# Kernel optimization log

Measured on AMD Instinct MI355X. Metric: run time of the kernel, lower is better.

## Reference

```python
import jax, jax.numpy as jnp
import numpy as np

SYM_LIST = np.array([12, 15, 18, 19, 20], dtype=np.int32)   # symmetric class ids (dataset.get_sym_list())
SELECT_ID = np.arange(1, 31, dtype=np.int32)                 # self.select_id = [1..30]
STEP = 20                                                     # pixel subsampling stride
SCORING_WEIGHT = 0.01


def quat_to_mat(q):
    """Exact translation of get_loss.quaternion_matrix. q: [..., 4] -> [..., 3, 3]."""
    q0, q1, q2, q3 = q[..., 0], q[..., 1], q[..., 2], q[..., 3]
    R = jnp.stack([
        1.0 - 2.0 * (q2 ** 2 + q3 ** 2), 2.0 * q1 * q2 - 2.0 * q0 * q3, 2.0 * q0 * q2 + 2.0 * q1 * q3,
        2.0 * q1 * q2 + 2.0 * q3 * q0, 1.0 - 2.0 * (q1 ** 2 + q3 ** 2), -2.0 * q0 * q1 + 2.0 * q2 * q3,
        -2.0 * q0 * q2 + 2.0 * q1 * q3, 2.0 * q0 * q1 + 2.0 * q2 * q3, 1.0 - 2.0 * (q1 ** 2 + q2 ** 2),
    ], axis=-1)
    return R.reshape(q.shape[:-1] + (3, 3))


def setup_inputs() -> dict:
    key = jax.random.key(0)
    ks = jax.random.split(key, 7)
    bs, h, w, P = 8, 64, 64, 400
    pred_r = jax.random.normal(ks[0], (bs, 4, h, w), jnp.float32)
    pred_t = jax.random.normal(ks[1], (bs, 3, h, w), jnp.float32) * 0.1
    pred_score = jax.random.uniform(ks[2], (bs, h, w), jnp.float32, 1e-3, 1.0)
    gt_r = jax.random.normal(ks[3], (bs, 3, 3), jnp.float32)
    gt_t = jax.random.normal(ks[4], (bs, 3), jnp.float32) * 0.1
    cls_ids = jax.random.randint(ks[5], (bs,), 0, 30, jnp.int32)
    model_xyz = jax.random.normal(ks[6], (bs, 3, P), jnp.float32) * 0.05
    return {"pred_r": pred_r, "pred_t": pred_t, "pred_score": pred_score,
            "gt_r": gt_r, "gt_t": gt_t, "cls_ids": cls_ids, "model_xyz": model_xyz}


def reference(pred_r, pred_t, pred_score, gt_r, gt_t, cls_ids, model_xyz):
    bs, _, h, w = pred_r.shape
    hw = h * w
    # per-pixel quaternion normalization
    pred_r = pred_r / jnp.linalg.norm(pred_r, axis=1, keepdims=True)
    pr = pred_r.reshape(bs, 4, hw)
    pt = pred_t.reshape(bs, 3, hw)
    ps = pred_score.reshape(bs, hw)
    # static strided subsampling of valid pixels (full mask -> every STEP-th pixel)
    V = hw // STEP
    idx = jnp.arange(V) * STEP
    pr = pr[:, :, idx]                 # [bs,4,V]
    pt = pt[:, :, idx]                 # [bs,3,V]
    ps = ps[:, idx]                    # [bs,V]
    R_pre = quat_to_mat(jnp.moveaxis(pr, 1, 2))                       # [bs,V,3,3]
    # transformed model points per valid pixel
    pred = jnp.einsum('bvij,bjp->bvip', R_pre, model_xyz) \
        + jnp.moveaxis(pt, 1, 2)[..., None]                           # [bs,V,3,P]
    gt = jnp.einsum('bij,bjp->bip', gt_r, model_xyz) + gt_t[..., None]  # [bs,3,P]
    # ADD: same-index point distances
    add = jnp.mean(jnp.linalg.norm(pred - gt[:, None], axis=2), axis=2)  # [bs,V]
    # ADD-S: nearest-neighbor (knn_one_point + gather == min over gt points)
    pn = jnp.sum(pred ** 2, axis=2)                                    # [bs,V,P]
    gn = jnp.sum(gt ** 2, axis=1)                                      # [bs,P]
    cross = jnp.einsum('bvip,biq->bvpq', pred, gt)                     # [bs,V,P,P]
    d2 = pn[..., None] + gn[:, None, None, :] - 2.0 * cross
    adds = jnp.mean(jnp.sqrt(jnp.maximum(jnp.min(d2, axis=-1), 0.0)), axis=2)  # [bs,V]
    is_sym = jnp.isin(cls_ids, jnp.asarray(SYM_LIST))                  # [bs]
    add_ij = jnp.where(is_sym[:, None], adds, add)                     # [bs,V]
    valid = jnp.isin(cls_ids + 1, jnp.asarray(SELECT_ID))              # cls+1 in select_id
    sub_value = jnp.where(valid, jnp.mean(add_ij, axis=1), 0.0)
    sub_loss = jnp.where(valid,
                         jnp.mean(add_ij * ps - SCORING_WEIGHT * jnp.log(ps), axis=1), 0.0)
    gadd_loss = jnp.mean(sub_loss)
    gadd = jnp.mean(sub_value)
    bad = jnp.isinf(gadd_loss) | jnp.isnan(gadd_loss)
    gadd_loss = jnp.where(bad, 0.0, gadd_loss)
    return gadd_loss + 0.0 * gadd
```

## Files before the change

kernel.cpp:

```cpp
#include <hip/hip_runtime.h>
#include <math.h>

#define NP 400
#define NV 204
#define STEP 20
#define HW 4096
#define BS 8
#define NBLK (NV * BS)

__global__ __launch_bounds__(512) void partial_kernel(
    const float* __restrict__ pred_r,
    const float* __restrict__ pred_t,
    const float* __restrict__ pred_score,
    const float* __restrict__ gt_r,
    const float* __restrict__ gt_t,
    const int*   __restrict__ cls_ids,
    const float* __restrict__ model_xyz,
    float* __restrict__ partials)
{
    const int v   = blockIdx.x;
    const int b   = blockIdx.y;
    const int tid = threadIdx.x;
    const int pix = v * STEP;

    __shared__ float4 s_g[NP];
    __shared__ float  s_part[8];

    const int   cls = cls_ids[b];
    const bool  sym = (cls==12)||(cls==15)||(cls==18)||(cls==19)||(cls==20);
    const bool  valid = (cls+1 >= 1) && (cls+1 <= 30);

    const float* mb = model_xyz + (size_t)b * 3 * NP;

    if (tid < NP) {
        const float g00 = gt_r[b*9+0], g01 = gt_r[b*9+1], g02 = gt_r[b*9+2];
        const float g10 = gt_r[b*9+3], g11 = gt_r[b*9+4], g12 = gt_r[b*9+5];
        const float g20 = gt_r[b*9+6], g21 = gt_r[b*9+7], g22 = gt_r[b*9+8];
        const float gtx = gt_t[b*3+0], gty = gt_t[b*3+1], gtz = gt_t[b*3+2];
        float mx = mb[tid], my = mb[NP+tid], mz = mb[2*NP+tid];
        s_g[tid] = make_float4(g00*mx + g01*my + g02*mz + gtx,
                               g10*mx + g11*my + g12*mz + gty,
                               g20*mx + g21*my + g22*mz + gtz, 0.0f);
    }

    float q0 = pred_r[((size_t)b*4+0)*HW + pix];
    float q1 = pred_r[((size_t)b*4+1)*HW + pix];
    float q2 = pred_r[((size_t)b*4+2)*HW + pix];
    float q3 = pred_r[((size_t)b*4+3)*HW + pix];
    {
        float inv = 1.0f / sqrtf(q0*q0 + q1*q1 + q2*q2 + q3*q3);
        q0 *= inv; q1 *= inv; q2 *= inv; q3 *= inv;
    }
    const float R00 = 1.0f - 2.0f*(q2*q2 + q3*q3);
    const float R01 = 2.0f*q1*q2 - 2.0f*q0*q3;
    const float R02 = 2.0f*q0*q2 + 2.0f*q1*q3;
    const float R10 = 2.0f*q1*q2 + 2.0f*q3*q0;
    const float R11 = 1.0f - 2.0f*(q1*q1 + q3*q3);
    const float R12 = -2.0f*q0*q1 + 2.0f*q2*q3;
    const float R20 = -2.0f*q0*q2 + 2.0f*q1*q3;
    const float R21 = 2.0f*q0*q1 + 2.0f*q2*q3;
    const float R22 = 1.0f - 2.0f*(q1*q1 + q2*q2);

    const float ptx = pred_t[((size_t)b*3+0)*HW + pix];
    const float pty = pred_t[((size_t)b*3+1)*HW + pix];
    const float ptz = pred_t[((size_t)b*3+2)*HW + pix];

    __syncthreads();

    float local = 0.0f;
    if (tid < NP) {
        const int p = tid;
        float mx = mb[p], my = mb[NP+p], mz = mb[2*NP+p];
        float px = R00*mx + R01*my + R02*mz + ptx;
        float py = R10*mx + R11*my + R12*mz + pty;
        float pz = R20*mx + R21*my + R22*mz + ptz;
        float d2;
        if (sym) {
            float m0 = 3.4e38f, m1 = 3.4e38f, m2 = 3.4e38f, m3 = 3.4e38f;
            for (int q = 0; q < NP; q += 4) {
                float4 g0 = s_g[q+0], g1 = s_g[q+1], g2 = s_g[q+2], g3 = s_g[q+3];
                float dx0 = px-g0.x, dy0 = py-g0.y, dz0 = pz-g0.z;
                float dx1 = px-g1.x, dy1 = py-g1.y, dz1 = pz-g1.z;
                float dx2 = px-g2.x, dy2 = py-g2.y, dz2 = pz-g2.z;
                float dx3 = px-g3.x, dy3 = py-g3.y, dz3 = pz-g3.z;
                m0 = fminf(m0, dx0*dx0 + dy0*dy0 + dz0*dz0);
                m1 = fminf(m1, dx1*dx1 + dy1*dy1 + dz1*dz1);
                m2 = fminf(m2, dx2*dx2 + dy2*dy2 + dz2*dz2);
                m3 = fminf(m3, dx3*dx3 + dy3*dy3 + dz3*dz3);
            }
            d2 = fminf(fminf(m0, m1), fminf(m2, m3));
        } else {
            float4 g = s_g[p];
            float dx = px-g.x, dy = py-g.y, dz = pz-g.z;
            d2 = dx*dx + dy*dy + dz*dz;
        }
        local = sqrtf(d2);
    }

    #pragma unroll
    for (int off = 32; off > 0; off >>= 1)
        local += __shfl_down(local, off, 64);
    const int wave = tid >> 6;
    if ((tid & 63) == 0) s_part[wave] = local;
    __syncthreads();
    if (tid == 0) {
        float tot = 0.0f;
        #pragma unroll
        for (int w = 0; w < 8; ++w) tot += s_part[w];
        float mean = tot * (1.0f / NP);
        float ps   = pred_score[(size_t)b*HW + pix];
        float c = 0.0f;
        if (valid)
            c = (mean * ps - 0.01f * logf(ps)) * (1.0f / NBLK);
        partials[b * NV + v] = c;
    }
}

__global__ __launch_bounds__(256) void finalize_kernel(
    const float* __restrict__ partials, float* __restrict__ out)
{
    __shared__ float s_part[4];
    const int tid = threadIdx.x;
    float local = 0.0f;
    for (int i = tid; i < NBLK; i += 256) local += partials[i];
    #pragma unroll
    for (int off = 32; off > 0; off >>= 1)
        local += __shfl_down(local, off, 64);
    if ((tid & 63) == 0) s_part[tid >> 6] = local;
    __syncthreads();
    if (tid == 0) {
        float vv = s_part[0] + s_part[1] + s_part[2] + s_part[3];
        if (isnan(vv) || isinf(vv)) vv = 0.0f;
        out[0] = vv;
    }
}

extern "C" void kernel_launch(void* const* d_in, const int* in_sizes, int n_in,
                              void* d_out, int out_size, void* d_ws, size_t ws_size,
                              hipStream_t stream) {
    const float* pred_r     = (const float*)d_in[0];
    const float* pred_t     = (const float*)d_in[1];
    const float* pred_score = (const float*)d_in[2];
    const float* gt_r       = (const float*)d_in[3];
    const float* gt_t       = (const float*)d_in[4];
    const int*   cls_ids    = (const int*)d_in[5];
    const float* model_xyz  = (const float*)d_in[6];
    float* out      = (float*)d_out;
    float* partials = (float*)d_ws;

    dim3 grid(NV, BS);
    partial_kernel<<<grid, 512, 0, stream>>>(pred_r, pred_t, pred_score,
                                             gt_r, gt_t, cls_ids, model_xyz, partials);
    finalize_kernel<<<1, 256, 0, stream>>>(partials, out);
}
```

Measured before the change: 71.74 us.

## Process two model points per thread with SoA shared layout and 256-thread blocks

Shrinks each block from 512 to 256 threads, so each thread now handles two predicted points and every vectorized shared-memory load of ground-truth points is reused across both. The ground-truth points are stored as separate x/y/z arrays, so four points come in with three float4 loads and no padding lane. Before, 112 of the 512 threads did no work. The finalize kernel now reads the partials as float4. The cost is lower occupancy per block and a thread-load imbalance, since only 144 of the 256 threads have a second point.

```diff
diff --git a/kernel.cpp b/kernel.cpp
--- a/kernel.cpp
+++ b/kernel.cpp
@@ -8,7 +8,7 @@
 #define BS 8
 #define NBLK (NV * BS)
 
-__global__ __launch_bounds__(512) void partial_kernel(
+__global__ __launch_bounds__(256) void partial_kernel(
     const float* __restrict__ pred_r,
     const float* __restrict__ pred_t,
     const float* __restrict__ pred_score,
@@ -23,24 +23,27 @@
     const int tid = threadIdx.x;
     const int pix = v * STEP;
 
-    __shared__ float4 s_g[NP];
-    __shared__ float  s_part[8];
+    __shared__ float s_gx[NP], s_gy[NP], s_gz[NP];
+    __shared__ float s_part[4];
 
     const int   cls = cls_ids[b];
     const bool  sym = (cls==12)||(cls==15)||(cls==18)||(cls==19)||(cls==20);
     const bool  valid = (cls+1 >= 1) && (cls+1 <= 30);
+    const bool  has2 = (tid < NP - 256);
 
     const float* mb = model_xyz + (size_t)b * 3 * NP;
 
-    if (tid < NP) {
+    {
         const float g00 = gt_r[b*9+0], g01 = gt_r[b*9+1], g02 = gt_r[b*9+2];
         const float g10 = gt_r[b*9+3], g11 = gt_r[b*9+4], g12 = gt_r[b*9+5];
         const float g20 = gt_r[b*9+6], g21 = gt_r[b*9+7], g22 = gt_r[b*9+8];
         const float gtx = gt_t[b*3+0], gty = gt_t[b*3+1], gtz = gt_t[b*3+2];
-        float mx = mb[tid], my = mb[NP+tid], mz = mb[2*NP+tid];
-        s_g[tid] = make_float4(g00*mx + g01*my + g02*mz + gtx,
-                               g10*mx + g11*my + g12*mz + gty,
-                               g20*mx + g21*my + g22*mz + gtz, 0.0f);
+        for (int q = tid; q < NP; q += 256) {
+            float mx = mb[q], my = mb[NP+q], mz = mb[2*NP+q];
+            s_gx[q] = g00*mx + g01*my + g02*mz + gtx;
+            s_gy[q] = g10*mx + g11*my + g12*mz + gty;
+            s_gz[q] = g20*mx + g21*my + g22*mz + gtz;
+        }
     }
 
     float q0 = pred_r[((size_t)b*4+0)*HW + pix];
@@ -67,35 +70,55 @@
 
     __syncthreads();
 
-    float local = 0.0f;
-    if (tid < NP) {
-        const int p = tid;
-        float mx = mb[p], my = mb[NP+p], mz = mb[2*NP+p];
-        float px = R00*mx + R01*my + R02*mz + ptx;
-        float py = R10*mx + R11*my + R12*mz + pty;
-        float pz = R20*mx + R21*my + R22*mz + ptz;
-        float d2;
-        if (sym) {
-            float m0 = 3.4e38f, m1 = 3.4e38f, m2 = 3.4e38f, m3 = 3.4e38f;
-            for (int q = 0; q < NP; q += 4) {
-                float4 g0 = s_g[q+0], g1 = s_g[q+1], g2 = s_g[q+2], g3 = s_g[q+3];
-                float dx0 = px-g0.x, dy0 = py-g0.y, dz0 = pz-g0.z;
-                float dx1 = px-g1.x, dy1 = py-g1.y, dz1 = pz-g1.z;
-                float dx2 = px-g2.x, dy2 = py-g2.y, dz2 = pz-g2.z;
-                float dx3 = px-g3.x, dy3 = py-g3.y, dz3 = pz-g3.z;
-                m0 = fminf(m0, dx0*dx0 + dy0*dy0 + dz0*dz0);
-                m1 = fminf(m1, dx1*dx1 + dy1*dy1 + dz1*dz1);
-                m2 = fminf(m2, dx2*dx2 + dy2*dy2 + dz2*dz2);
-                m3 = fminf(m3, dx3*dx3 + dy3*dy3 + dz3*dz3);
+    const int p0 = tid;
+    const int p1 = has2 ? tid + 256 : tid;
+    float mx0 = mb[p0], my0 = mb[NP+p0], mz0 = mb[2*NP+p0];
+    float mx1 = mb[p1], my1 = mb[NP+p1], mz1 = mb[2*NP+p1];
+    const float px0 = R00*mx0 + R01*my0 + R02*mz0 + ptx;
+    const float py0 = R10*mx0 + R11*my0 + R12*mz0 + pty;
+    const float pz0 = R20*mx0 + R21*my0 + R22*mz0 + ptz;
+    const float px1 = R00*mx1 + R01*my1 + R02*mz1 + ptx;
+    const float py1 = R10*mx1 + R11*my1 + R12*mz1 + pty;
+    const float pz1 = R20*mx1 + R21*my1 + R22*mz1 + ptz;
+
+    float d2_0, d2_1;
+    if (sym) {
+        float a0 = 3.4e38f, a1 = 3.4e38f, a2 = 3.4e38f, a3 = 3.4e38f;
+        float b0 = 3.4e38f, b1 = 3.4e38f, b2 = 3.4e38f, b3 = 3.4e38f;
+        for (int q = 0; q < NP; q += 4) {
+            const float4 gx = *reinterpret_cast<const float4*>(&s_gx[q]);
+            const float4 gy = *reinterpret_cast<const float4*>(&s_gy[q]);
+            const float4 gz = *reinterpret_cast<const float4*>(&s_gz[q]);
+            {
+                float dx = px0-gx.x, dy = py0-gy.x, dz = pz0-gz.x;
+                a0 = fminf(a0, dx*dx + dy*dy + dz*dz);
+                dx = px0-gx.y; dy = py0-gy.y; dz = pz0-gz.y;
+                a1 = fminf(a1, dx*dx + dy*dy + dz*dz);
+                dx = px0-gx.z; dy = py0-gy.z; dz = pz0-gz.z;
+                a2 = fminf(a2, dx*dx + dy*dy + dz*dz);
+                dx = px0-gx.w; dy = py0-gy.w; dz = pz0-gz.w;
+                a3 = fminf(a3, dx*dx + dy*dy + dz*dz);
             }
-            d2 = fminf(fminf(m0, m1), fminf(m2, m3));
-        } else {
-            float4 g = s_g[p];
-            float dx = px-g.x, dy = py-g.y, dz = pz-g.z;
-            d2 = dx*dx + dy*dy + dz*dz;
+            {
+                float dx = px1-gx.x, dy = py1-gy.x, dz = pz1-gz.x;
+                b0 = fminf(b0, dx*dx + dy*dy + dz*dz);
+                dx = px1-gx.y; dy = py1-gy.y; dz = pz1-gz.y;
+                b1 = fminf(b1, dx*dx + dy*dy + dz*dz);
+                dx = px1-gx.z; dy = py1-gy.z; dz = pz1-gz.z;
+                b2 = fminf(b2, dx*dx + dy*dy + dz*dz);
+                dx = px1-gx.w; dy = py1-gy.w; dz = pz1-gz.w;
+                b3 = fminf(b3, dx*dx + dy*dy + dz*dz);
+            }
         }
-        local = sqrtf(d2);
+        d2_0 = fminf(fminf(a0, a1), fminf(a2, a3));
+        d2_1 = fminf(fminf(b0, b1), fminf(b2, b3));
+    } else {
+        float dx = px0 - s_gx[p0], dy = py0 - s_gy[p0], dz = pz0 - s_gz[p0];
+        d2_0 = dx*dx + dy*dy + dz*dz;
+        dx = px1 - s_gx[p1]; dy = py1 - s_gy[p1]; dz = pz1 - s_gz[p1];
+        d2_1 = dx*dx + dy*dy + dz*dz;
     }
+    float local = sqrtf(d2_0) + (has2 ? sqrtf(d2_1) : 0.0f);
 
     #pragma unroll
     for (int off = 32; off > 0; off >>= 1)
@@ -104,9 +127,7 @@
     if ((tid & 63) == 0) s_part[wave] = local;
     __syncthreads();
     if (tid == 0) {
-        float tot = 0.0f;
-        #pragma unroll
-        for (int w = 0; w < 8; ++w) tot += s_part[w];
+        float tot  = s_part[0] + s_part[1] + s_part[2] + s_part[3];
         float mean = tot * (1.0f / NP);
         float ps   = pred_score[(size_t)b*HW + pix];
         float c = 0.0f;
@@ -121,8 +142,12 @@
 {
     __shared__ float s_part[4];
     const int tid = threadIdx.x;
+    const float4* p4 = reinterpret_cast<const float4*>(partials);
     float local = 0.0f;
-    for (int i = tid; i < NBLK; i += 256) local += partials[i];
+    for (int i = tid; i < NBLK / 4; i += 256) {
+        float4 vv = p4[i];
+        local += vv.x + vv.y + vv.z + vv.w;
+    }
     #pragma unroll
     for (int off = 32; off > 0; off >>= 1)
         local += __shfl_down(local, off, 64);
@@ -149,7 +174,7 @@
     float* partials = (float*)d_ws;
 
     dim3 grid(NV, BS);
-    partial_kernel<<<grid, 512, 0, stream>>>(pred_r, pred_t, pred_score,
+    partial_kernel<<<grid, 256, 0, stream>>>(pred_r, pred_t, pred_score,
                                              gt_r, gt_t, cls_ids, model_xyz, partials);
     finalize_kernel<<<1, 256, 0, stream>>>(partials, out);
 }
```

Result: faster. 69.99 us (-2.4%).

## Register-tile nearest-neighbor search with expanded-norm distances across four waves

Applied to the files above, without the earlier changes.

Shrinks blocks to 256 threads. Each lane now holds 7 predicted points in registers, and each wave scans a quarter of the ground-truth points using the expanded distance form -2p·g + |g|^2, computed as three FMAs. Per-wave minima are merged through shared memory. This cuts shared-memory loads per distance and reduces the ALU work in the symmetric kNN loop. In exchange it adds register pressure, padding lanes that do clamped redundant work, and an extra barrier. The finalize kernel is also switched to float4 loads.

```diff
diff --git a/kernel.cpp b/kernel.cpp
--- a/kernel.cpp
+++ b/kernel.cpp
@@ -7,8 +7,9 @@
 #define HW 4096
 #define BS 8
 #define NBLK (NV * BS)
+#define NJ 7
 
-__global__ __launch_bounds__(512) void partial_kernel(
+__global__ __launch_bounds__(256) void partial_kernel(
     const float* __restrict__ pred_r,
     const float* __restrict__ pred_t,
     const float* __restrict__ pred_score,
@@ -18,13 +19,15 @@
     const float* __restrict__ model_xyz,
     float* __restrict__ partials)
 {
-    const int v   = blockIdx.x;
-    const int b   = blockIdx.y;
-    const int tid = threadIdx.x;
-    const int pix = v * STEP;
+    const int v    = blockIdx.x;
+    const int b    = blockIdx.y;
+    const int tid  = threadIdx.x;
+    const int lane = tid & 63;
+    const int wave = tid >> 6;
+    const int pix  = v * STEP;
 
     __shared__ float4 s_g[NP];
-    __shared__ float  s_part[8];
+    __shared__ float  s_wmin[4][NP];
 
     const int   cls = cls_ids[b];
     const bool  sym = (cls==12)||(cls==15)||(cls==18)||(cls==19)||(cls==20);
@@ -32,15 +35,18 @@
 
     const float* mb = model_xyz + (size_t)b * 3 * NP;
 
-    if (tid < NP) {
+    {
         const float g00 = gt_r[b*9+0], g01 = gt_r[b*9+1], g02 = gt_r[b*9+2];
         const float g10 = gt_r[b*9+3], g11 = gt_r[b*9+4], g12 = gt_r[b*9+5];
         const float g20 = gt_r[b*9+6], g21 = gt_r[b*9+7], g22 = gt_r[b*9+8];
         const float gtx = gt_t[b*3+0], gty = gt_t[b*3+1], gtz = gt_t[b*3+2];
-        float mx = mb[tid], my = mb[NP+tid], mz = mb[2*NP+tid];
-        s_g[tid] = make_float4(g00*mx + g01*my + g02*mz + gtx,
-                               g10*mx + g11*my + g12*mz + gty,
-                               g20*mx + g21*my + g22*mz + gtz, 0.0f);
+        for (int q = tid; q < NP; q += 256) {
+            float mx = mb[q], my = mb[NP+q], mz = mb[2*NP+q];
+            float gx = g00*mx + g01*my + g02*mz + gtx;
+            float gy = g10*mx + g11*my + g12*mz + gty;
+            float gz = g20*mx + g21*my + g22*mz + gtz;
+            s_g[q] = make_float4(gx, gy, gz, gx*gx + gy*gy + gz*gz);
+        }
     }
 
     float q0 = pred_r[((size_t)b*4+0)*HW + pix];
@@ -65,54 +71,85 @@
     const float pty = pred_t[((size_t)b*3+1)*HW + pix];
     const float ptz = pred_t[((size_t)b*3+2)*HW + pix];
 
+    float px[NJ], py[NJ], pz[NJ], nx[NJ], ny[NJ], nz[NJ], pn[NJ];
+    #pragma unroll
+    for (int j = 0; j < NJ; ++j) {
+        int p  = lane + 64*j;
+        int pc = (p < NP) ? p : (NP - 1);
+        float mx = mb[pc], my = mb[NP+pc], mz = mb[2*NP+pc];
+        float x = R00*mx + R01*my + R02*mz + ptx;
+        float y = R10*mx + R11*my + R12*mz + pty;
+        float z = R20*mx + R21*my + R22*mz + ptz;
+        px[j] = x; py[j] = y; pz[j] = z;
+        nx[j] = -2.0f*x; ny[j] = -2.0f*y; nz[j] = -2.0f*z;
+        pn[j] = x*x + y*y + z*z;
+    }
+
     __syncthreads();
 
     float local = 0.0f;
-    if (tid < NP) {
-        const int p = tid;
-        float mx = mb[p], my = mb[NP+p], mz = mb[2*NP+p];
-        float px = R00*mx + R01*my + R02*mz + ptx;
-        float py = R10*mx + R11*my + R12*mz + pty;
-        float pz = R20*mx + R21*my + R22*mz + ptz;
-        float d2;
-        if (sym) {
-            float m0 = 3.4e38f, m1 = 3.4e38f, m2 = 3.4e38f, m3 = 3.4e38f;
-            for (int q = 0; q < NP; q += 4) {
-                float4 g0 = s_g[q+0], g1 = s_g[q+1], g2 = s_g[q+2], g3 = s_g[q+3];
-                float dx0 = px-g0.x, dy0 = py-g0.y, dz0 = pz-g0.z;
-                float dx1 = px-g1.x, dy1 = py-g1.y, dz1 = pz-g1.z;
-                float dx2 = px-g2.x, dy2 = py-g2.y, dz2 = pz-g2.z;
-                float dx3 = px-g3.x, dy3 = py-g3.y, dz3 = pz-g3.z;
-                m0 = fminf(m0, dx0*dx0 + dy0*dy0 + dz0*dz0);
-                m1 = fminf(m1, dx1*dx1 + dy1*dy1 + dz1*dz1);
-                m2 = fminf(m2, dx2*dx2 + dy2*dy2 + dz2*dz2);
-                m3 = fminf(m3, dx3*dx3 + dy3*dy3 + dz3*dz3);
+    if (sym) {
+        float m[NJ];
+        #pragma unroll
+        for (int j = 0; j < NJ; ++j) m[j] = 3.4e38f;
+        const int qbase = wave * 100;
+        for (int i = 0; i < 25; ++i) {
+            const float4 g0 = s_g[qbase + 4*i + 0];
+            const float4 g1 = s_g[qbase + 4*i + 1];
+            const float4 g2 = s_g[qbase + 4*i + 2];
+            const float4 g3 = s_g[qbase + 4*i + 3];
+            #pragma unroll
+            for (int j = 0; j < NJ; ++j) {
+                m[j] = fminf(m[j], fmaf(nx[j], g0.x, fmaf(ny[j], g0.y, fmaf(nz[j], g0.z, g0.w))));
+                m[j] = fminf(m[j], fmaf(nx[j], g1.x, fmaf(ny[j], g1.y, fmaf(nz[j], g1.z, g1.w))));
+                m[j] = fminf(m[j], fmaf(nx[j], g2.x, fmaf(ny[j], g2.y, fmaf(nz[j], g2.z, g2.w))));
+                m[j] = fminf(m[j], fmaf(nx[j], g3.x, fmaf(ny[j], g3.y, fmaf(nz[j], g3.z, g3.w))));
             }
-            d2 = fminf(fminf(m0, m1), fminf(m2, m3));
-        } else {
-            float4 g = s_g[p];
-            float dx = px-g.x, dy = py-g.y, dz = pz-g.z;
-            d2 = dx*dx + dy*dy + dz*dz;
         }
-        local = sqrtf(d2);
+        #pragma unroll
+        for (int j = 0; j < NJ; ++j) {
+            int p = lane + 64*j;
+            if (p < NP) s_wmin[wave][p] = m[j];
+        }
+        __syncthreads();
+        if (wave == 0) {
+            #pragma unroll
+            for (int j = 0; j < NJ; ++j) {
+                int p = lane + 64*j;
+                if (p < NP) {
+                    float mm = fminf(fminf(s_wmin[0][p], s_wmin[1][p]),
+                                     fminf(s_wmin[2][p], s_wmin[3][p]));
+                    float d2 = fmaxf(pn[j] + mm, 0.0f);
+                    local += sqrtf(d2);
+                }
+            }
+        }
+    } else {
+        if (wave == 0) {
+            #pragma unroll
+            for (int j = 0; j < NJ; ++j) {
+                int p = lane + 64*j;
+                if (p < NP) {
+                    float4 g = s_g[p];
+                    float dx = px[j]-g.x, dy = py[j]-g.y, dz = pz[j]-g.z;
+                    local += sqrtf(dx*dx + dy*dy + dz*dz);
+                }
+            }
+        }
     }
 
-    #pragma unroll
-    for (int off = 32; off > 0; off >>= 1)
-        local += __shfl_down(local, off, 64);
-    const int wave = tid >> 6;
-    if ((tid & 63) == 0) s_part[wave] = local;
-    __syncthreads();
-    if (tid == 0) {
-        float tot = 0.0f;
+    if (wave == 0) {
         #pragma unroll
-        for (int w = 0; w < 8; ++w) tot += s_part[w];
-        float mean = tot * (1.0f / NP);
-        float ps   = pred_score[(size_t)b*HW + pix];
-        float c = 0.0f;
-        if (valid)
-            c = (mean * ps - 0.01f * logf(ps)) * (1.0f / NBLK);
-        partials[b * NV + v] = c;
+        for (int off = 32; off > 0; off >>= 1)
+            local += __shfl_down(local, off, 64);
+        if (lane == 0) {
+            float mean = local * (1.0f / NP);
+            float ps   = pred_score[(size_t)b*HW + pix];
+            float c = 0.0f;
+            if (valid)
+                c = (mean * ps - 0.01f * logf(ps)) * (1.0f / NBLK);
+            partials[b * NV + v] = c;
+        }
     }
 }
 
@@ -121,8 +158,12 @@
 {
     __shared__ float s_part[4];
     const int tid = threadIdx.x;
+    const float4* p4 = reinterpret_cast<const float4*>(partials);
     float local = 0.0f;
-    for (int i = tid; i < NBLK; i += 256) local += partials[i];
+    for (int i = tid; i < NBLK / 4; i += 256) {
+        float4 vv = p4[i];
+        local += vv.x + vv.y + vv.z + vv.w;
+    }
     #pragma unroll
     for (int off = 32; off > 0; off >>= 1)
         local += __shfl_down(local, off, 64);
@@ -149,7 +190,7 @@
     float* partials = (float*)d_ws;
 
     dim3 grid(NV, BS);
-    partial_kernel<<<grid, 512, 0, stream>>>(pred_r, pred_t, pred_score,
+    partial_kernel<<<grid, 256, 0, stream>>>(pred_r, pred_t, pred_score,
                                              gt_r, gt_t, cls_ids, model_xyz, partials);
     finalize_kernel<<<1, 256, 0, stream>>>(partials, out);
 }
```

Measured after the change: 70.77 us. About the same (-1.4%).
